# Optimization experiments

Measured on AMD Instinct MI355X. Metric: run time of the kernel, lower is better.

The kernel has to match this reference:

```python
import jax, jax.numpy as jnp
import numpy as np
import math

GH, GW = 14, 14            # hw_shape
L = GH * GW                # 196 tokens
NUM_POINTS = 4
NUM_NODES = 4 * NUM_POINTS # 16 interpolation nodes (4 directions x 4 points)
B, H, DH = 32, 12, 64      # batch, num_heads, head_dim


def build_spatial_extension_table():
    """Dense [L, L, NUM_NODES] table, faithful to build_spatial_extension."""
    T = np.zeros((L, L, NUM_NODES), dtype=np.float32)
    curve_length = GH
    for rank in range(L):
        h, w = divmod(rank, GW)
        for step in range(1, curve_length):
            interp = (NUM_POINTS - 1) * (step - 1) / (curve_length - 1)
            si = int(interp)
            dist = math.exp(-step ** 2 / curve_length ** 2)
            sd = dist * (1.0 - (interp - si))
            nd = dist * (interp - si)
            # top / bottom move along h (same w); left / right along w (same h)
            if h - step >= 0:
                p = rank - step * GW
                T[rank, p, 0 * NUM_POINTS + si] += sd
                T[rank, p, 0 * NUM_POINTS + si + 1] += nd
            if h + step < GH:
                p = rank + step * GW
                T[rank, p, 1 * NUM_POINTS + si] += sd
                T[rank, p, 1 * NUM_POINTS + si + 1] += nd
            if w - step >= 0:
                p = rank - step
                T[rank, p, 2 * NUM_POINTS + si] += sd
                T[rank, p, 2 * NUM_POINTS + si + 1] += nd
            if w + step < GW:
                p = rank + step
                T[rank, p, 3 * NUM_POINTS + si] += sd
                T[rank, p, 3 * NUM_POINTS + si + 1] += nd
    return T


def setup_inputs() -> dict:
    key = jax.random.key(0)
    k1, k2, k3 = jax.random.split(key, 3)
    x = jax.random.normal(k1, (B, H, L, DH), dtype=jnp.float32)
    table = jnp.asarray(build_spatial_extension_table())
    # per-order learnable params (init_parameters_base): [num_nodes, head_dim, num_heads]
    param_1 = jax.random.normal(k2, (NUM_NODES, DH, H), dtype=jnp.float32) * 0.02
    param_2 = jax.random.normal(k3, (NUM_NODES, DH, H), dtype=jnp.float32) * 0.02
    return {"x": x, "table": table, "param_1": param_1, "param_2": param_2}


def reference(x, table, param_1, param_2):
    # SAVE aggregation: trans = anchor(identity over [L,L] x [DH,H])
    #                         + sum_orders einsum('mnk,kdh->mndh', table, param_o)
    # out[b,h,m,d] = sum_n trans[m,n,d,h] * x[b,h,n,d]
    # Anchor term == x itself; compute the spatial terms without materializing
    # the [L,L,DH,H] dense aggregation tensor.
    # _param_norm is identity for extension mode (num_orders == 2).
    agg1 = jnp.einsum('mnk,kdh,bhnd->bhmd', table, param_1, x)
    agg2 = jnp.einsum('mnk,kdh,bhnd->bhmd', table, param_2, x)
    return x + agg1 + agg2
```

## Files before the change

kernel.cpp:

```cpp
#include <hip/hip_runtime.h>


#define GH 14
#define GW 14
#define LL 196
#define DH 64
#define NH 12

__global__ __launch_bounds__(256, 3)
void save_kernel(const float* __restrict__ x,
                 const float* __restrict__ p1,
                 const float* __restrict__ p2,
                 float* __restrict__ out)
{
    const int bh  = blockIdx.x >> 1;
    const int dq  = blockIdx.x & 1;
    const int h   = bh % NH;
    const int tid = threadIdx.x;
    const int dl  = tid & 31;
    const int slot = tid >> 5;
    const int d   = dq * 32 + dl;

    __shared__ float xs[LL * 32];
    __shared__ float ps[LL * 32];

    const float* xb = x + (size_t)bh * (LL * DH) + dq * 32;
    for (int idx = tid; idx < LL * 8; idx += 256) {
        const int n = idx >> 3, q = idx & 7;
        const float4 v = *reinterpret_cast<const float4*>(xb + n * DH + q * 4);
        *reinterpret_cast<float4*>(&xs[n * 32 + q * 4]) = v;
    }

    float P[16];
    #pragma unroll
    for (int k = 0; k < 16; ++k) {
        const int off = k * (DH * NH) + d * NH + h;
        P[k] = p1[off] + p2[off];
    }
    float Qr[26], Qc[26];
    #pragma unroll
    for (int t = 0; t < 13; ++t) {
        const int   s    = t + 1;
        const int   si   = (3 * t) / 13;
        const float frac = (3.0f * (float)t) / 13.0f - (float)si;
        const float dist = expf(-(float)(s * s) / 196.0f);
        const float sd = dist * (1.0f - frac);
        const float nd = dist * frac;
        Qr[t]      = sd * P[si]      + nd * P[si + 1];
        Qr[13 + t] = sd * P[4 + si]  + nd * P[4 + si + 1];
        Qc[t]      = sd * P[8 + si]  + nd * P[8 + si + 1];
        Qc[13 + t] = sd * P[12 + si] + nd * P[12 + si + 1];
    }

    __syncthreads();

    for (int w = slot; w < GW; w += 8) {
        float xcol[GH];
        #pragma unroll
        for (int j = 0; j < GH; ++j) xcol[j] = xs[(j * GW + w) * 32 + dl];
        #pragma unroll
        for (int i = 0; i < GH; ++i) {
            float a = xcol[i];
            #pragma unroll
            for (int j = 0; j < GH; ++j) {
                if (j == i) continue;
                const float q = (j < i) ? Qr[i - j - 1] : Qr[12 + j - i];
                a += q * xcol[j];
            }
            ps[(i * GW + w) * 32 + dl] = a;
        }
    }

    __syncthreads();

    float* og = out + (size_t)bh * (LL * DH) + dq * 32;
    for (int r = slot; r < GH; r += 8) {
        float xrow[GW];
        #pragma unroll
        for (int j = 0; j < GW; ++j) xrow[j] = xs[(r * GW + j) * 32 + dl];
        #pragma unroll
        for (int i = 0; i < GW; ++i) {
            float a = 0.0f;
            #pragma unroll
            for (int j = 0; j < GW; ++j) {
                if (j == i) continue;
                const float q = (j < i) ? Qc[i - j - 1] : Qc[12 + j - i];
                a += q * xrow[j];
            }
            const int n = r * GW + i;
            og[n * DH + dl] = ps[n * 32 + dl] + a;
        }
    }
}

extern "C" void kernel_launch(void* const* d_in, const int* in_sizes, int n_in,
                              void* d_out, int out_size, void* d_ws, size_t ws_size,
                              hipStream_t stream) {
    const float* x  = (const float*)d_in[0];
    const float* p1 = (const float*)d_in[2];
    const float* p2 = (const float*)d_in[3];
    float* out = (float*)d_out;

    dim3 grid(32 * 12 * 2);
    dim3 block(256);
    save_kernel<<<grid, block, 0, stream>>>(x, p1, p2, out);
}
```

Measured before the change: 85.10 us.

## Split head dim into 16-wide slices so every thread owns one column/row

Each block now handles 16 head-dim channels instead of 32, and the grid becomes 384x4 blocks. With 16 threads per row slot, all 14 column and row slots run in a single pass instead of two uneven passes. The Qc coefficients are computed after the column pass to lower register pressure, and launch bounds are raised to 6 blocks per CU. The trade-off is 16-float (64-byte) segments for global loads and stores, 2 of 16 warps-slots idle, and the parameter-mixing work repeated across twice as many blocks.

```diff
diff --git a/kernel.cpp b/kernel.cpp
--- a/kernel.cpp
+++ b/kernel.cpp
@@ -6,58 +6,58 @@
 #define LL 196
 #define DH 64
 #define NH 12
+#define DL 16
 
-__global__ __launch_bounds__(256, 3)
+__global__ __launch_bounds__(256, 6)
 void save_kernel(const float* __restrict__ x,
                  const float* __restrict__ p1,
                  const float* __restrict__ p2,
                  float* __restrict__ out)
 {
-    const int bh  = blockIdx.x >> 1;
-    const int dq  = blockIdx.x & 1;
-    const int h   = bh % NH;
-    const int tid = threadIdx.x;
-    const int dl  = tid & 31;
-    const int slot = tid >> 5;
-    const int d   = dq * 32 + dl;
+    const int bh   = blockIdx.x;
+    const int dq   = blockIdx.y;
+    const int h    = bh % NH;
+    const int tid  = threadIdx.x;
+    const int dl   = tid & (DL - 1);
+    const int slot = tid >> 4;
+    const int d    = dq * DL + dl;
 
-    __shared__ float xs[LL * 32];
-    __shared__ float ps[LL * 32];
+    __shared__ float xs[LL * DL];
+    __shared__ float ps[LL * DL];
 
-    const float* xb = x + (size_t)bh * (LL * DH) + dq * 32;
-    for (int idx = tid; idx < LL * 8; idx += 256) {
-        const int n = idx >> 3, q = idx & 7;
+    const float* xb = x + (size_t)bh * (LL * DH) + dq * DL;
+    for (int idx = tid; idx < LL * 4; idx += 256) {
+        const int n = idx >> 2, q = idx & 3;
         const float4 v = *reinterpret_cast<const float4*>(xb + n * DH + q * 4);
-        *reinterpret_cast<float4*>(&xs[n * 32 + q * 4]) = v;
+        *reinterpret_cast<float4*>(&xs[n * DL + q * 4]) = v;
     }
 
-    float P[16];
-    #pragma unroll
-    for (int k = 0; k < 16; ++k) {
-        const int off = k * (DH * NH) + d * NH + h;
-        P[k] = p1[off] + p2[off];
-    }
-    float Qr[26], Qc[26];
-    #pragma unroll
-    for (int t = 0; t < 13; ++t) {
-        const int   s    = t + 1;
-        const int   si   = (3 * t) / 13;
-        const float frac = (3.0f * (float)t) / 13.0f - (float)si;
-        const float dist = expf(-(float)(s * s) / 196.0f);
-        const float sd = dist * (1.0f - frac);
-        const float nd = dist * frac;
-        Qr[t]      = sd * P[si]      + nd * P[si + 1];
-        Qr[13 + t] = sd * P[4 + si]  + nd * P[4 + si + 1];
-        Qc[t]      = sd * P[8 + si]  + nd * P[8 + si + 1];
-        Qc[13 + t] = sd * P[12 + si] + nd * P[12 + si + 1];
+    const int poff = d * NH + h;
+    float Qr[26];
+    {
+        float P[8];
+        #pragma unroll
+        for (int k = 0; k < 8; ++k)
+            P[k] = p1[k * (DH * NH) + poff] + p2[k * (DH * NH) + poff];
+        #pragma unroll
+        for (int t = 0; t < 13; ++t) {
+            const int   s    = t + 1;
+            const int   si   = (3 * t) / 13;
+            const float frac = (3.0f * (float)t) / 13.0f - (float)si;
+            const float dist = expf(-(float)(s * s) / 196.0f);
+            const float sd = dist * (1.0f - frac), nd = dist * frac;
+            Qr[t]      = sd * P[si]     + nd * P[si + 1];
+            Qr[13 + t] = sd * P[4 + si] + nd * P[4 + si + 1];
+        }
     }
 
     __syncthreads();
 
-    for (int w = slot; w < GW; w += 8) {
+    if (slot < GW) {
+        const int w = slot;
         float xcol[GH];
         #pragma unroll
-        for (int j = 0; j < GH; ++j) xcol[j] = xs[(j * GW + w) * 32 + dl];
+        for (int j = 0; j < GH; ++j) xcol[j] = xs[(j * GW + w) * DL + dl];
         #pragma unroll
         for (int i = 0; i < GH; ++i) {
             float a = xcol[i];
@@ -67,28 +67,46 @@
                 const float q = (j < i) ? Qr[i - j - 1] : Qr[12 + j - i];
                 a += q * xcol[j];
             }
-            ps[(i * GW + w) * 32 + dl] = a;
+            ps[(i * GW + w) * DL + dl] = a;
+        }
+    }
+
+    float Qc[26];
+    {
+        float P[8];
+        #pragma unroll
+        for (int k = 0; k < 8; ++k)
+            P[k] = p1[(8 + k) * (DH * NH) + poff] + p2[(8 + k) * (DH * NH) + poff];
+        #pragma unroll
+        for (int t = 0; t < 13; ++t) {
+            const int   s    = t + 1;
+            const int   si   = (3 * t) / 13;
+            const float frac = (3.0f * (float)t) / 13.0f - (float)si;
+            const float dist = expf(-(float)(s * s) / 196.0f);
+            const float sd = dist * (1.0f - frac), nd = dist * frac;
+            Qc[t]      = sd * P[si]     + nd * P[si + 1];
+            Qc[13 + t] = sd * P[4 + si] + nd * P[4 + si + 1];
         }
     }
 
     __syncthreads();
 
-    float* og = out + (size_t)bh * (LL * DH) + dq * 32;
-    for (int r = slot; r < GH; r += 8) {
+    if (slot < GH) {
+        const int r = slot;
+        float* og = out + (size_t)bh * (LL * DH) + dq * DL;
         float xrow[GW];
         #pragma unroll
-        for (int j = 0; j < GW; ++j) xrow[j] = xs[(r * GW + j) * 32 + dl];
+        for (int j = 0; j < GW; ++j) xrow[j] = xs[(r * GW + j) * DL + dl];
         #pragma unroll
         for (int i = 0; i < GW; ++i) {
-            float a = 0.0f;
+            float a = ps[(r * GW + i) * DL + dl];
             #pragma unroll
             for (int j = 0; j < GW; ++j) {
                 if (j == i) continue;
                 const float q = (j < i) ? Qc[i - j - 1] : Qc[12 + j - i];
                 a += q * xrow[j];
             }
-            const int n = r * GW + i;
-            og[n * DH + dl] = ps[n * 32 + dl] + a;
+            og[(r * GW + i) * DH + dl] = a;
         }
     }
 }
@@ -101,7 +119,7 @@
     const float* p2 = (const float*)d_in[3];
     float* out = (float*)d_out;
 
-    dim3 grid(32 * 12 * 2);
+    dim3 grid(32 * 12, 4);
     dim3 block(256);
     save_kernel<<<grid, block, 0, stream>>>(x, p1, p2, out);
 }
```

New measurement: 86.28 us. No clear change (+1.4%).
